# Kernel tuning notes

Measured on AMD Instinct MI355X. Metric: run time of the kernel, lower is better.

The kernel has to match this reference:

```python
import jax, jax.numpy as jnp
import numpy as np

NUM_GRAPHS = 256
NUM_LAYERS = 4
HIDDEN = 256
N_FEATS = 9
VOCAB = 119
BN_EPS = 1e-5


def setup_inputs() -> dict:
    key = jax.random.key(0)
    ks = jax.random.split(key, 16)
    N, E, H = 10000, 320000, HIDDEN
    x = jax.random.randint(ks[0], (N, N_FEATS), 0, 2, dtype=jnp.int64)
    edge_index = jax.random.randint(ks[1], (2, E), 0, N, dtype=jnp.int64)
    batch_ids = jnp.sort(jax.random.randint(ks[2], (N,), 0, NUM_GRAPHS, dtype=jnp.int64))
    s = 1.0 / np.sqrt(H)
    emb = jax.random.normal(ks[3], (N_FEATS, VOCAB, H), jnp.float32) * 0.02
    W = jax.random.normal(ks[4], (NUM_LAYERS, H, H), jnp.float32) * s
    b = jnp.zeros((NUM_LAYERS, H), jnp.float32)
    gamma = jnp.ones((NUM_LAYERS, H), jnp.float32)
    beta = jnp.zeros((NUM_LAYERS, H), jnp.float32)
    mlp_W1 = jax.random.normal(ks[5], (H, H // 2), jnp.float32) * s
    mlp_b1 = jnp.zeros((H // 2,), jnp.float32)
    mlp_W2 = jax.random.normal(ks[6], (H // 2, H // 4), jnp.float32) * (1.0 / np.sqrt(H // 2))
    mlp_b2 = jnp.zeros((H // 4,), jnp.float32)
    mlp_W3 = jax.random.normal(ks[7], (H // 4, 1), jnp.float32) * (1.0 / np.sqrt(H // 4))
    mlp_b3 = jnp.zeros((1,), jnp.float32)
    return dict(x=x, edge_index=edge_index, batch_ids=batch_ids, emb=emb, W=W, b=b,
                gamma=gamma, beta=beta, mlp_W1=mlp_W1, mlp_b1=mlp_b1,
                mlp_W2=mlp_W2, mlp_b2=mlp_b2, mlp_W3=mlp_W3, mlp_b3=mlp_b3)


def reference(x, edge_index, batch_ids, emb, W, b, gamma, beta,
              mlp_W1, mlp_b1, mlp_W2, mlp_b2, mlp_W3, mlp_b3):
    N = x.shape[0]
    src, dst = edge_index[0], edge_index[1]

    # AtomEncoder: sum of per-feature embeddings. emb[f, x[:,f]] -> [N, 9, H]
    h = jnp.sum(emb[jnp.arange(N_FEATS), x], axis=1)

    # GCN normalization with self-loops: deg_i = 1 + in-degree, norm = deg^-1/2
    deg = 1.0 + jax.ops.segment_sum(jnp.ones_like(dst, jnp.float32), dst, num_segments=N)
    nrm = jax.lax.rsqrt(deg)
    edge_w = (nrm[src] * nrm[dst])[:, None]   # [E,1]
    self_w = (nrm * nrm)[:, None]             # [N,1]

    for l in range(NUM_LAYERS):
        identity = h
        hw = h @ W[l]                                     # dense GEMM [N,H]x[H,H]
        agg = jax.ops.segment_sum(hw[src] * edge_w, dst, num_segments=N) + hw * self_w
        h = agg + b[l]
        # BatchNorm1d (training statistics over nodes)
        mu = jnp.mean(h, axis=0)
        var = jnp.var(h, axis=0)
        h = (h - mu) * jax.lax.rsqrt(var + BN_EPS) * gamma[l] + beta[l]
        h = jax.nn.relu(h)
        h = h + identity  # residual

    # global mean pool over graph ids
    sums = jax.ops.segment_sum(h, batch_ids, num_segments=NUM_GRAPHS)
    cnt = jax.ops.segment_sum(jnp.ones((N,), jnp.float32), batch_ids, num_segments=NUM_GRAPHS)
    g = sums / jnp.maximum(cnt, 1.0)[:, None]             # [G, H]

    # MLP head [H, H/2, H/4, 1]
    g = jax.nn.relu(g @ mlp_W1 + mlp_b1)
    g = jax.nn.relu(g @ mlp_W2 + mlp_b2)
    return g @ mlp_W3 + mlp_b3
```

## Files before the change

### kernel.cpp

```cpp
#include <hip/hip_runtime.h>

#define HID 256
#define NFEAT 9
#define VOCAB 119
#define NLAYERS 4
#define NGRAPHS 256
#define BN_EPS 1e-5f
#define POISON 0xAAAAAAAAu
#define CAP 128

typedef short short8 __attribute__((ext_vector_type(8)));
typedef float floatx4 __attribute__((ext_vector_type(4)));

__device__ inline unsigned short f2bf(float f) {
    unsigned int u = __float_as_uint(f);
    unsigned int r = u + 0x7FFF + ((u >> 16) & 1);
    return (unsigned short)(r >> 16);
}
__device__ inline float bf2f(unsigned short u) {
    return __uint_as_float(((unsigned int)u) << 16);
}

__global__ __launch_bounds__(256) void setup_misc(
        const int* __restrict__ x, const float* __restrict__ emb,
        const float* __restrict__ W, const int* __restrict__ src,
        const int* __restrict__ dst,
        int* __restrict__ fillc, int* __restrict__ bucket,
        unsigned short* __restrict__ wt, unsigned short* __restrict__ hbA,
        int N, int E, int nbFill) {
    const int bx = blockIdx.x;
    const int tid = threadIdx.x;
    __shared__ float sw[32][33];
    __shared__ int xf[NFEAT];

    if (bx < nbFill) {
        int i = bx * 256 + tid;
        if (i < E) {
            int d = dst[i];
            int slot = (int)((unsigned)atomicAdd(&fillc[d], 1) - POISON);
            if (slot < CAP) bucket[(size_t)d * CAP + slot] = src[i];
        }
    } else if (bx < nbFill + 256) {
        int j = bx - nbFill;
        int l = j >> 6;
        int rem = j & 63;
        int k0 = (rem >> 3) * 32, n0 = (rem & 7) * 32;
        int c = tid & 31, r8 = tid >> 5;
        const float* Wl = W + (size_t)l * HID * HID;
        unsigned short* Wtl = wt + (size_t)l * HID * HID;
#pragma unroll
        for (int p = 0; p < 4; ++p) {
            int r = r8 + p * 8;
            sw[r][c] = Wl[(k0 + r) * HID + n0 + c];
        }
        __syncthreads();
#pragma unroll
        for (int p = 0; p < 4; ++p) {
            int r = r8 + p * 8;
            Wtl[(size_t)(n0 + r) * HID + k0 + c] = f2bf(sw[c][r]);
        }
    } else {
        int n = bx - nbFill - 256;
        if (n < N) {
            if (tid < NFEAT) xf[tid] = x[n * NFEAT + tid];
            __syncthreads();
            float s = 0.f;
#pragma unroll
            for (int f = 0; f < NFEAT; ++f) s += emb[(size_t)(f * VOCAB + xf[f]) * HID + tid];
            hbA[(size_t)n * HID + tid] = f2bf(s);
        }
    }
}

__global__ __launch_bounds__(256) void agg_g4_kernel(const unsigned short* __restrict__ hb,
                                                     const int* __restrict__ fillc,
                                                     const int* __restrict__ bucket,
                                                     unsigned short* __restrict__ aggb, int N) {
    int bx = blockIdx.x;
    int half = bx & 1;
    int tid = threadIdx.x;
    int wave = tid >> 6;
    int lane = tid & 63;
    int g = lane >> 4;
    int sl = lane & 15;
    int n = (bx >> 1) * 4 + wave;
    if (n >= N) return;
    int co = half * 128 + sl * 8;
    const unsigned short* hbc = hb + co;
    int len = (int)((unsigned)fillc[n] - POISON);
    float nd = rsqrtf(1.0f + (float)len);
    int lenc = min(len, CAP);
    size_t bbase = (size_t)n * CAP;
    float a[8];
#pragma unroll
    for (int k = 0; k < 8; ++k) a[k] = 0.f;

    int done = 0;
    while (done < lenc) {
        int m = min(64, lenc - done);
        int li = done + (lane < m ? lane : m - 1);
        int sE = bucket[bbase + li];
        int dgs = (int)((unsigned)fillc[sE] - POISON);
        float wl = rsqrtf(1.0f + (float)dgs) * nd;
        int mq = m & ~3;
        int j = 0;
        for (; j < mq; j += 4) {
            int jj = j + g;
            int srcn = __shfl(sE, jj, 64);
            float w = __shfl(wl, jj, 64);
            short8 u = *(const short8*)&hbc[(size_t)srcn * HID];
#pragma unroll
            for (int k = 0; k < 8; ++k) a[k] += w * bf2f((unsigned short)u[k]);
        }
        if (j < m) {
            int jj = j + g;
            int cj = jj < m ? jj : (m - 1);
            int srcn = __shfl(sE, cj, 64);
            float w = __shfl(wl, cj, 64);
            if (jj >= m) w = 0.f;
            short8 u = *(const short8*)&hbc[(size_t)srcn * HID];
#pragma unroll
            for (int k = 0; k < 8; ++k) a[k] += w * bf2f((unsigned short)u[k]);
        }
        done += m;
    }
#pragma unroll
    for (int k = 0; k < 8; ++k) {
        a[k] += __shfl_xor(a[k], 16);
        a[k] += __shfl_xor(a[k], 32);
    }
    if (g == 0) {
        float sw2 = nd * nd;
        short8 us = *(const short8*)&hbc[(size_t)n * HID];
        short8 o;
#pragma unroll
        for (int k = 0; k < 8; ++k) {
            float v = a[k] + sw2 * bf2f((unsigned short)us[k]);
            o[k] = (short)f2bf(v);
        }
        *(short8*)&aggb[(size_t)n * HID + co] = o;
    }
}

__global__ __launch_bounds__(256) void mfma_gemm128(const unsigned short* __restrict__ A,
                                                    const unsigned short* __restrict__ Bt,
                                                    const float* __restrict__ bias,
                                                    unsigned short* __restrict__ C,
                                                    float* __restrict__ sums, int M) {
    __shared__ unsigned short As[128][40];
    __shared__ unsigned short Bs[64][40];
    __shared__ float lsum[64];
    __shared__ float lsq[64];
    int tid = threadIdx.x;
    int row0 = blockIdx.x * 128;
    int col0 = blockIdx.y * 64;
    int lane = tid & 63;
    int wid = tid >> 6;
    int arow = tid >> 1;
    int akc = (tid & 1) * 16;
    int brow = tid >> 2;
    int bkc = (tid & 3) * 8;
    int wm = (wid & 1) * 64;
    int wn = (wid >> 1) * 32;
    int quad = lane >> 4;
    int ln = lane & 15;

    floatx4 acc[4][2];
#pragma unroll
    for (int r = 0; r < 4; ++r)
#pragma unroll
        for (int c = 0; c < 2; ++c) acc[r][c] = (floatx4){0.f, 0.f, 0.f, 0.f};

    if (tid < 64) { lsum[tid] = 0.f; lsq[tid] = 0.f; }

    for (int kk = 0; kk < HID; kk += 32) {
        short8 av0 = {0, 0, 0, 0, 0, 0, 0, 0};
        short8 av1 = {0, 0, 0, 0, 0, 0, 0, 0};
        int ar = row0 + arow;
        if (ar < M) {
            av0 = *(const short8*)&A[(size_t)ar * HID + kk + akc];
            av1 = *(const short8*)&A[(size_t)ar * HID + kk + akc + 8];
        }
        short8 bv = *(const short8*)&Bt[(size_t)(col0 + brow) * HID + kk + bkc];
        *(short8*)&As[arow][akc] = av0;
        *(short8*)&As[arow][akc + 8] = av1;
        *(short8*)&Bs[brow][bkc] = bv;
        __syncthreads();
        short8 bf0 = *(const short8*)&Bs[wn + ln][quad * 8];
        short8 bf1 = *(const short8*)&Bs[wn + 16 + ln][quad * 8];
#pragma unroll
        for (int r = 0; r < 4; ++r) {
            short8 af = *(const short8*)&As[wm + r * 16 + ln][quad * 8];
            acc[r][0] = __builtin_amdgcn_mfma_f32_16x16x32_bf16(af, bf0, acc[r][0], 0, 0, 0);
            acc[r][1] = __builtin_amdgcn_mfma_f32_16x16x32_bf16(af, bf1, acc[r][1], 0, 0, 0);
        }
        __syncthreads();
    }
    float bias0 = bias[col0 + wn + ln];
    float bias1 = bias[col0 + wn + 16 + ln];
    float p0 = 0.f, q0 = 0.f, p1 = 0.f, q1 = 0.f;
#pragma unroll
    for (int r = 0; r < 4; ++r) {
#pragma unroll
        for (int rr = 0; rr < 4; ++rr) {
            int row = row0 + wm + r * 16 + quad * 4 + rr;
            if (row < M) {
                float v0 = acc[r][0][rr] + bias0;
                float v1 = acc[r][1][rr] + bias1;
                C[(size_t)row * HID + col0 + wn + ln] = f2bf(v0);
                C[(size_t)row * HID + col0 + wn + 16 + ln] = f2bf(v1);
                p0 += v0; q0 += v0 * v0;
                p1 += v1; q1 += v1 * v1;
            }
        }
    }
    atomicAdd(&lsum[wn + ln], p0);
    atomicAdd(&lsq[wn + ln], q0);
    atomicAdd(&lsum[wn + 16 + ln], p1);
    atomicAdd(&lsq[wn + 16 + ln], q1);
    __syncthreads();
    if (tid < 64) {
        unsafeAtomicAdd(&sums[col0 + tid], lsum[tid]);
        unsafeAtomicAdd(&sums[HID + col0 + tid], lsq[tid]);
    }
}

__global__ __launch_bounds__(256) void bn_kernel(const unsigned short* __restrict__ hwb,
                                                 const float* __restrict__ sums,
                                                 const float* __restrict__ gamma,
                                                 const float* __restrict__ beta,
                                                 const unsigned short* __restrict__ hold,
                                                 unsigned short* __restrict__ hbnew, int N) {
    int i4 = blockIdx.x * blockDim.x + threadIdx.x;
    int base = i4 * 4;
    if (base >= N * HID) return;
    int c = base & (HID - 1);
    float invN = 1.0f / (float)N;
    float4 s4 = *(const float4*)&sums[c];
    float4 q4 = *(const float4*)&sums[HID + c];
    float4 g4 = *(const float4*)&gamma[c];
    float4 be4 = *(const float4*)&beta[c];
    ushort4 v = *(const ushort4*)&hwb[base];
    ushort4 r = *(const ushort4*)&hold[base];
    ushort4 o;
    {
        float mu = s4.x * invN, var = q4.x * invN - mu * mu;
        o.x = f2bf(fmaxf((bf2f(v.x) - mu) * g4.x * rsqrtf(var + BN_EPS) + be4.x, 0.f) + bf2f(r.x));
        mu = s4.y * invN; var = q4.y * invN - mu * mu;
        o.y = f2bf(fmaxf((bf2f(v.y) - mu) * g4.y * rsqrtf(var + BN_EPS) + be4.y, 0.f) + bf2f(r.y));
        mu = s4.z * invN; var = q4.z * invN - mu * mu;
        o.z = f2bf(fmaxf((bf2f(v.z) - mu) * g4.z * rsqrtf(var + BN_EPS) + be4.z, 0.f) + bf2f(r.z));
        mu = s4.w * invN; var = q4.w * invN - mu * mu;
        o.w = f2bf(fmaxf((bf2f(v.w) - mu) * g4.w * rsqrtf(var + BN_EPS) + be4.w, 0.f) + bf2f(r.w));
    }
    *(ushort4*)&hbnew[base] = o;
}

__device__ inline int lower_bound_g(const int* __restrict__ a, int n, int key) {
    int lo = 0, hi = n;
    while (lo < hi) {
        int mid = (lo + hi) >> 1;
        if (a[mid] < key) lo = mid + 1; else hi = mid;
    }
    return lo;
}

__global__ __launch_bounds__(256) void pool_mlp_bn_kernel(
        const unsigned short* __restrict__ hwb,
        const float* __restrict__ sums,
        const float* __restrict__ gamma,
        const float* __restrict__ beta,
        const unsigned short* __restrict__ resid,
        const int* __restrict__ batch, int N,
        const float* __restrict__ W1, const float* __restrict__ b1,
        const float* __restrict__ W2, const float* __restrict__ b2,
        const float* __restrict__ W3, const float* __restrict__ b3,
        float* __restrict__ out) {
    int g = blockIdx.x, tid = threadIdx.x;
    int lo = lower_bound_g(batch, N, g);
    int hi = lower_bound_g(batch, N, g + 1);
    float invN = 1.0f / (float)N;
    float mu = sums[tid] * invN;
    float var = sums[HID + tid] * invN - mu * mu;
    float sc = gamma[tid] * rsqrtf(var + BN_EPS);
    float be = beta[tid];
    float s = 0.f;
    for (int i = lo; i < hi; ++i) {
        float v = (bf2f(hwb[(size_t)i * HID + tid]) - mu) * sc + be;
        v = fmaxf(v, 0.f) + bf2f(resid[(size_t)i * HID + tid]);
        s += v;
    }
    __shared__ float gs[256];
    __shared__ float t1[128];
    __shared__ float t2[64];
    float inv = 1.0f / fmaxf((float)(hi - lo), 1.0f);
    gs[tid] = s * inv;
    __syncthreads();
    if (tid < 128) {
        float a = b1[tid];
        for (int k = 0; k < 256; ++k) a += gs[k] * W1[k * 128 + tid];
        t1[tid] = fmaxf(a, 0.f);
    }
    __syncthreads();
    if (tid < 64) {
        float a = b2[tid];
        for (int k = 0; k < 128; ++k) a += t1[k] * W2[k * 64 + tid];
        t2[tid] = fmaxf(a, 0.f);
    }
    __syncthreads();
    if (tid < 64) {
        float p = t2[tid] * W3[tid];
#pragma unroll
        for (int off = 32; off >= 1; off >>= 1) p += __shfl_down(p, off);
        if (tid == 0) out[g] = p + b3[0];
    }
}

extern "C" void kernel_launch(void* const* d_in, const int* in_sizes, int n_in,
                              void* d_out, int out_size, void* d_ws, size_t ws_size,
                              hipStream_t stream) {
    const int* x      = (const int*)d_in[0];
    const int* ei     = (const int*)d_in[1];
    const int* batch  = (const int*)d_in[2];
    const float* emb  = (const float*)d_in[3];
    const float* W    = (const float*)d_in[4];
    const float* b    = (const float*)d_in[5];
    const float* gamma= (const float*)d_in[6];
    const float* beta = (const float*)d_in[7];
    const float* W1   = (const float*)d_in[8];
    const float* b1   = (const float*)d_in[9];
    const float* W2   = (const float*)d_in[10];
    const float* b2   = (const float*)d_in[11];
    const float* W3   = (const float*)d_in[12];
    const float* b3   = (const float*)d_in[13];
    float* out = (float*)d_out;

    int N = in_sizes[0] / NFEAT;
    int E = in_sizes[1] / 2;
    const int* srcp = ei;
    const int* dstp = ei + E;

    char* ws = (char*)d_ws;
    auto alloc = [&](size_t bytes) -> char* {
        char* p = ws;
        ws += (bytes + 255) & ~(size_t)255;
        return p;
    };
    int* fillc    = (int*)alloc((size_t)N * 4);
    int* bucket   = (int*)alloc((size_t)N * CAP * 4);
    unsigned short* hbA  = (unsigned short*)alloc((size_t)N * HID * 2);
    unsigned short* hbB  = (unsigned short*)alloc((size_t)N * HID * 2);
    unsigned short* aggb = (unsigned short*)alloc((size_t)N * HID * 2);
    unsigned short* hwb  = (unsigned short*)alloc((size_t)N * HID * 2);
    unsigned short* wt   = (unsigned short*)alloc((size_t)NLAYERS * HID * HID * 2);
    float* bnsums = (float*)alloc((size_t)NLAYERS * 2 * HID * 4);

    int nbFill = (E + 255) / 256;
    int miscGrid = nbFill + 256 + N;
    setup_misc<<<miscGrid, 256, 0, stream>>>(x, emb, W, srcp, dstp, fillc, bucket, wt, hbA,
                                             N, E, nbFill);

    unsigned short* hbcur = hbA;
    unsigned short* hboth = hbB;
    int aggGrid = ((N + 3) / 4) * 2;
    for (int l = 0; l < NLAYERS; ++l) {
        float* lsums = bnsums + (size_t)l * 2 * HID;
        agg_g4_kernel<<<aggGrid, 256, 0, stream>>>(hbcur, fillc, bucket, aggb, N);
        dim3 ggrid((N + 127) / 128, 4);
        mfma_gemm128<<<ggrid, 256, 0, stream>>>(aggb, wt + (size_t)l * HID * HID,
                                                b + (size_t)l * HID, hwb, lsums, N);
        if (l < NLAYERS - 1) {
            bn_kernel<<<((size_t)N * HID / 4 + 255) / 256, 256, 0, stream>>>(
                hwb, lsums, gamma + (size_t)l * HID, beta + (size_t)l * HID,
                hbcur, hboth, N);
            unsigned short* tb = hbcur; hbcur = hboth; hboth = tb;
        }
    }

    pool_mlp_bn_kernel<<<NGRAPHS, 256, 0, stream>>>(
        hwb, bnsums + (size_t)3 * 2 * HID, gamma + (size_t)3 * HID, beta + (size_t)3 * HID,
        hbcur, batch, N, W1, b1, W2, b2, W3, b3, out);
}
```

Before: 271.3 us.

## Fuse BatchNorm, ReLU and residual into GEMM epilogue via grid-wide column barrier

The separate BatchNorm kernel is removed. The GEMM now accumulates the column statistics, waits at a spin barrier until every row block of its column tile has contributed, then applies normalization, ReLU and the residual directly from its accumulators before writing the new hidden state. The bias add is also dropped, because batch-norm mean subtraction cancels it. This saves an extra read-write pass over the hidden activations and one launch per layer. In exchange, all blocks must be co-resident, which `launch_bounds(256,2)` is meant to ensure, and the barrier counter assumes the workspace starts at the poison value without being reset in-kernel.

```diff
diff --git a/kernel.cpp b/kernel.cpp
--- a/kernel.cpp
+++ b/kernel.cpp
@@ -142,11 +142,16 @@
     }
 }
 
-__global__ __launch_bounds__(256) void mfma_gemm128(const unsigned short* __restrict__ A,
-                                                    const unsigned short* __restrict__ Bt,
-                                                    const float* __restrict__ bias,
-                                                    unsigned short* __restrict__ C,
-                                                    float* __restrict__ sums, int M) {
+template <bool APPLY>
+__global__ __launch_bounds__(256, 2) void mfma_gemm_bn(
+        const unsigned short* __restrict__ A,
+        const unsigned short* __restrict__ Bt,
+        unsigned short* __restrict__ C,
+        float* __restrict__ sums,
+        const float* __restrict__ gamma,
+        const float* __restrict__ beta,
+        const unsigned short* __restrict__ resid,
+        int* __restrict__ cnt, int M) {
     __shared__ unsigned short As[128][40];
     __shared__ unsigned short Bs[64][40];
     __shared__ float lsum[64];
@@ -196,8 +201,8 @@
         }
         __syncthreads();
     }
-    float bias0 = bias[col0 + wn + ln];
-    float bias1 = bias[col0 + wn + 16 + ln];
+    const int c0 = col0 + wn + ln;
+    const int c1 = col0 + wn + 16 + ln;
     float p0 = 0.f, q0 = 0.f, p1 = 0.f, q1 = 0.f;
 #pragma unroll
     for (int r = 0; r < 4; ++r) {
@@ -205,10 +210,12 @@
         for (int rr = 0; rr < 4; ++rr) {
             int row = row0 + wm + r * 16 + quad * 4 + rr;
             if (row < M) {
-                float v0 = acc[r][0][rr] + bias0;
-                float v1 = acc[r][1][rr] + bias1;
-                C[(size_t)row * HID + col0 + wn + ln] = f2bf(v0);
-                C[(size_t)row * HID + col0 + wn + 16 + ln] = f2bf(v1);
+                float v0 = acc[r][0][rr];
+                float v1 = acc[r][1][rr];
+                if (!APPLY) {
+                    C[(size_t)row * HID + c0] = f2bf(v0);
+                    C[(size_t)row * HID + c1] = f2bf(v1);
+                }
                 p0 += v0; q0 += v0 * v0;
                 p1 += v1; q1 += v1 * v1;
             }
@@ -223,37 +230,43 @@
         unsafeAtomicAdd(&sums[col0 + tid], lsum[tid]);
         unsafeAtomicAdd(&sums[HID + col0 + tid], lsq[tid]);
     }
-}
-
-__global__ __launch_bounds__(256) void bn_kernel(const unsigned short* __restrict__ hwb,
-                                                 const float* __restrict__ sums,
-                                                 const float* __restrict__ gamma,
-                                                 const float* __restrict__ beta,
-                                                 const unsigned short* __restrict__ hold,
-                                                 unsigned short* __restrict__ hbnew, int N) {
-    int i4 = blockIdx.x * blockDim.x + threadIdx.x;
-    int base = i4 * 4;
-    if (base >= N * HID) return;
-    int c = base & (HID - 1);
-    float invN = 1.0f / (float)N;
-    float4 s4 = *(const float4*)&sums[c];
-    float4 q4 = *(const float4*)&sums[HID + c];
-    float4 g4 = *(const float4*)&gamma[c];
-    float4 be4 = *(const float4*)&beta[c];
-    ushort4 v = *(const ushort4*)&hwb[base];
-    ushort4 r = *(const ushort4*)&hold[base];
-    ushort4 o;
-    {
-        float mu = s4.x * invN, var = q4.x * invN - mu * mu;
-        o.x = f2bf(fmaxf((bf2f(v.x) - mu) * g4.x * rsqrtf(var + BN_EPS) + be4.x, 0.f) + bf2f(r.x));
-        mu = s4.y * invN; var = q4.y * invN - mu * mu;
-        o.y = f2bf(fmaxf((bf2f(v.y) - mu) * g4.y * rsqrtf(var + BN_EPS) + be4.y, 0.f) + bf2f(r.y));
-        mu = s4.z * invN; var = q4.z * invN - mu * mu;
-        o.z = f2bf(fmaxf((bf2f(v.z) - mu) * g4.z * rsqrtf(var + BN_EPS) + be4.z, 0.f) + bf2f(r.z));
-        mu = s4.w * invN; var = q4.w * invN - mu * mu;
-        o.w = f2bf(fmaxf((bf2f(v.w) - mu) * g4.w * rsqrtf(var + BN_EPS) + be4.w, 0.f) + bf2f(r.w));
-    }
-    *(ushort4*)&hbnew[base] = o;
+    if (APPLY) {
+        __syncthreads();
+        if (tid == 0) {
+            __threadfence();
+            atomicAdd(&cnt[blockIdx.y], 1);
+            unsigned target = gridDim.x;
+            while ((unsigned)__hip_atomic_load(&cnt[blockIdx.y], __ATOMIC_RELAXED,
+                                               __HIP_MEMORY_SCOPE_AGENT) - POISON < target)
+                __builtin_amdgcn_s_sleep(8);
+            __threadfence();
+        }
+        __syncthreads();
+        float invM = 1.0f / (float)M;
+        float s0 = __hip_atomic_load(&sums[c0], __ATOMIC_RELAXED, __HIP_MEMORY_SCOPE_AGENT);
+        float z0 = __hip_atomic_load(&sums[HID + c0], __ATOMIC_RELAXED, __HIP_MEMORY_SCOPE_AGENT);
+        float s1 = __hip_atomic_load(&sums[c1], __ATOMIC_RELAXED, __HIP_MEMORY_SCOPE_AGENT);
+        float z1 = __hip_atomic_load(&sums[HID + c1], __ATOMIC_RELAXED, __HIP_MEMORY_SCOPE_AGENT);
+        float mu0 = s0 * invM, var0 = z0 * invM - mu0 * mu0;
+        float mu1 = s1 * invM, var1 = z1 * invM - mu1 * mu1;
+        float sc0 = gamma[c0] * rsqrtf(var0 + BN_EPS), be0 = beta[c0];
+        float sc1 = gamma[c1] * rsqrtf(var1 + BN_EPS), be1 = beta[c1];
+#pragma unroll
+        for (int r = 0; r < 4; ++r) {
+#pragma unroll
+            for (int rr = 0; rr < 4; ++rr) {
+                int row = row0 + wm + r * 16 + quad * 4 + rr;
+                if (row < M) {
+                    float h0 = fmaxf((acc[r][0][rr] - mu0) * sc0 + be0, 0.f)
+                               + bf2f(resid[(size_t)row * HID + c0]);
+                    float h1 = fmaxf((acc[r][1][rr] - mu1) * sc1 + be1, 0.f)
+                               + bf2f(resid[(size_t)row * HID + c1]);
+                    C[(size_t)row * HID + c0] = f2bf(h0);
+                    C[(size_t)row * HID + c1] = f2bf(h1);
+                }
+            }
+        }
+    }
 }
 
 __device__ inline int lower_bound_g(const int* __restrict__ a, int n, int key) {
@@ -324,7 +337,6 @@
     const int* batch  = (const int*)d_in[2];
     const float* emb  = (const float*)d_in[3];
     const float* W    = (const float*)d_in[4];
-    const float* b    = (const float*)d_in[5];
     const float* gamma= (const float*)d_in[6];
     const float* beta = (const float*)d_in[7];
     const float* W1   = (const float*)d_in[8];
@@ -354,6 +366,7 @@
     unsigned short* hwb  = (unsigned short*)alloc((size_t)N * HID * 2);
     unsigned short* wt   = (unsigned short*)alloc((size_t)NLAYERS * HID * HID * 2);
     float* bnsums = (float*)alloc((size_t)NLAYERS * 2 * HID * 4);
+    int* cnt      = (int*)alloc((size_t)NLAYERS * 4 * 4);
 
     int nbFill = (E + 255) / 256;
     int miscGrid = nbFill + 256 + N;
@@ -363,17 +376,20 @@
     unsigned short* hbcur = hbA;
     unsigned short* hboth = hbB;
     int aggGrid = ((N + 3) / 4) * 2;
+    dim3 ggrid((N + 127) / 128, 4);
     for (int l = 0; l < NLAYERS; ++l) {
         float* lsums = bnsums + (size_t)l * 2 * HID;
         agg_g4_kernel<<<aggGrid, 256, 0, stream>>>(hbcur, fillc, bucket, aggb, N);
-        dim3 ggrid((N + 127) / 128, 4);
-        mfma_gemm128<<<ggrid, 256, 0, stream>>>(aggb, wt + (size_t)l * HID * HID,
-                                                b + (size_t)l * HID, hwb, lsums, N);
         if (l < NLAYERS - 1) {
-            bn_kernel<<<((size_t)N * HID / 4 + 255) / 256, 256, 0, stream>>>(
-                hwb, lsums, gamma + (size_t)l * HID, beta + (size_t)l * HID,
-                hbcur, hboth, N);
+            mfma_gemm_bn<true><<<ggrid, 256, 0, stream>>>(
+                aggb, wt + (size_t)l * HID * HID, hboth, lsums,
+                gamma + (size_t)l * HID, beta + (size_t)l * HID,
+                hbcur, cnt + l * 4, N);
             unsigned short* tb = hbcur; hbcur = hboth; hboth = tb;
+        } else {
+            mfma_gemm_bn<false><<<ggrid, 256, 0, stream>>>(
+                aggb, wt + (size_t)l * HID * HID, hwb, lsums,
+                nullptr, nullptr, nullptr, nullptr, N);
         }
     }
 
```

After: 323.2 us. 19.1% more time.

## Fuse all stages into one cooperative persistent kernel with grid syncs

Applied to the files above, without the earlier changes.

Replaces the sequence of separate launches (setup, per-layer aggregation, GEMM, batchnorm, pool+MLP) with one cooperative persistent kernel that loops over work units and separates stages with grid-wide syncs, falling back to the old launches if the cooperative launch fails. Shared memory is unioned across stages. This is meant to remove per-launch overhead and inter-kernel gaps. It also drops the bias add from the GEMM epilogue, which relies on batchnorm cancelling a per-column constant (the bias is zero in the test anyway). The risk is that grid syncs and a grid capped by occupancy limit parallelism in the gather and GEMM stages.

```diff
diff --git a/kernel.cpp b/kernel.cpp
--- a/kernel.cpp
+++ b/kernel.cpp
@@ -1,4 +1,7 @@
 #include <hip/hip_runtime.h>
+#include <hip/hip_cooperative_groups.h>
+
+namespace cg = cooperative_groups;
 
 #define HID 256
 #define NFEAT 9
@@ -21,69 +24,70 @@
     return __uint_as_float(((unsigned int)u) << 16);
 }
 
-__global__ __launch_bounds__(256) void setup_misc(
+struct SmemSetup { float sw[32][33]; int xf[NFEAT]; };
+struct SmemGemm  { unsigned short As[128][40]; unsigned short Bs[64][40];
+                   float lsum[64]; float lsq[64]; };
+struct SmemPool  { float gs[256]; float t1[128]; float t2[64]; };
+union SmemAll { SmemSetup s; SmemGemm g; SmemPool p; };
+
+__device__ inline void dev_setup_unit(int u, int tid,
         const int* __restrict__ x, const float* __restrict__ emb,
         const float* __restrict__ W, const int* __restrict__ src,
-        const int* __restrict__ dst,
-        int* __restrict__ fillc, int* __restrict__ bucket,
-        unsigned short* __restrict__ wt, unsigned short* __restrict__ hbA,
-        int N, int E, int nbFill) {
-    const int bx = blockIdx.x;
-    const int tid = threadIdx.x;
-    __shared__ float sw[32][33];
-    __shared__ int xf[NFEAT];
-
-    if (bx < nbFill) {
-        int i = bx * 256 + tid;
+        const int* __restrict__ dst, int* __restrict__ fillc,
+        int* __restrict__ bucket, unsigned short* __restrict__ wt,
+        unsigned short* __restrict__ hbA, int N, int E, int nbFill,
+        SmemSetup& sm) {
+    if (u < nbFill) {
+        int i = u * 256 + tid;
         if (i < E) {
             int d = dst[i];
             int slot = (int)((unsigned)atomicAdd(&fillc[d], 1) - POISON);
             if (slot < CAP) bucket[(size_t)d * CAP + slot] = src[i];
         }
-    } else if (bx < nbFill + 256) {
-        int j = bx - nbFill;
+    } else if (u < nbFill + 256) {
+        int j = u - nbFill;
         int l = j >> 6;
         int rem = j & 63;
         int k0 = (rem >> 3) * 32, n0 = (rem & 7) * 32;
         int c = tid & 31, r8 = tid >> 5;
         const float* Wl = W + (size_t)l * HID * HID;
         unsigned short* Wtl = wt + (size_t)l * HID * HID;
+        __syncthreads();
 #pragma unroll
         for (int p = 0; p < 4; ++p) {
             int r = r8 + p * 8;
-            sw[r][c] = Wl[(k0 + r) * HID + n0 + c];
+            sm.sw[r][c] = Wl[(k0 + r) * HID + n0 + c];
         }
         __syncthreads();
 #pragma unroll
         for (int p = 0; p < 4; ++p) {
             int r = r8 + p * 8;
-            Wtl[(size_t)(n0 + r) * HID + k0 + c] = f2bf(sw[c][r]);
+            Wtl[(size_t)(n0 + r) * HID + k0 + c] = f2bf(sm.sw[c][r]);
         }
     } else {
-        int n = bx - nbFill - 256;
+        int n = u - nbFill - 256;
         if (n < N) {
-            if (tid < NFEAT) xf[tid] = x[n * NFEAT + tid];
+            __syncthreads();
+            if (tid < NFEAT) sm.xf[tid] = x[n * NFEAT + tid];
             __syncthreads();
             float s = 0.f;
 #pragma unroll
-            for (int f = 0; f < NFEAT; ++f) s += emb[(size_t)(f * VOCAB + xf[f]) * HID + tid];
+            for (int f = 0; f < NFEAT; ++f)
+                s += emb[(size_t)(f * VOCAB + sm.xf[f]) * HID + tid];
             hbA[(size_t)n * HID + tid] = f2bf(s);
         }
     }
 }
 
-__global__ __launch_bounds__(256) void agg_g4_kernel(const unsigned short* __restrict__ hb,
-                                                     const int* __restrict__ fillc,
-                                                     const int* __restrict__ bucket,
-                                                     unsigned short* __restrict__ aggb, int N) {
-    int bx = blockIdx.x;
-    int half = bx & 1;
-    int tid = threadIdx.x;
+__device__ inline void dev_agg_unit(int u, int tid,
+        const unsigned short* __restrict__ hb, const int* __restrict__ fillc,
+        const int* __restrict__ bucket, unsigned short* __restrict__ aggb, int N) {
+    int half = u & 1;
     int wave = tid >> 6;
     int lane = tid & 63;
     int g = lane >> 4;
     int sl = lane & 15;
-    int n = (bx >> 1) * 4 + wave;
+    int n = (u >> 1) * 4 + wave;
     if (n >= N) return;
     int co = half * 128 + sl * 8;
     const unsigned short* hbc = hb + co;
@@ -108,9 +112,9 @@
             int jj = j + g;
             int srcn = __shfl(sE, jj, 64);
             float w = __shfl(wl, jj, 64);
-            short8 u = *(const short8*)&hbc[(size_t)srcn * HID];
-#pragma unroll
-            for (int k = 0; k < 8; ++k) a[k] += w * bf2f((unsigned short)u[k]);
+            short8 uvec = *(const short8*)&hbc[(size_t)srcn * HID];
+#pragma unroll
+            for (int k = 0; k < 8; ++k) a[k] += w * bf2f((unsigned short)uvec[k]);
         }
         if (j < m) {
             int jj = j + g;
@@ -118,9 +122,9 @@
             int srcn = __shfl(sE, cj, 64);
             float w = __shfl(wl, cj, 64);
             if (jj >= m) w = 0.f;
-            short8 u = *(const short8*)&hbc[(size_t)srcn * HID];
-#pragma unroll
-            for (int k = 0; k < 8; ++k) a[k] += w * bf2f((unsigned short)u[k]);
+            short8 uvec = *(const short8*)&hbc[(size_t)srcn * HID];
+#pragma unroll
+            for (int k = 0; k < 8; ++k) a[k] += w * bf2f((unsigned short)uvec[k]);
         }
         done += m;
     }
@@ -142,18 +146,12 @@
     }
 }
 
-__global__ __launch_bounds__(256) void mfma_gemm128(const unsigned short* __restrict__ A,
-                                                    const unsigned short* __restrict__ Bt,
-                                                    const float* __restrict__ bias,
-                                                    unsigned short* __restrict__ C,
-                                                    float* __restrict__ sums, int M) {
-    __shared__ unsigned short As[128][40];
-    __shared__ unsigned short Bs[64][40];
-    __shared__ float lsum[64];
-    __shared__ float lsq[64];
-    int tid = threadIdx.x;
-    int row0 = blockIdx.x * 128;
-    int col0 = blockIdx.y * 64;
+__device__ inline void dev_gemm_unit(int bxt, int by, int tid,
+        const unsigned short* __restrict__ A, const unsigned short* __restrict__ Bt,
+        unsigned short* __restrict__ C, float* __restrict__ sums,
+        SmemGemm& sm, int M) {
+    int row0 = bxt * 128;
+    int col0 = by * 64;
     int lane = tid & 63;
     int wid = tid >> 6;
     int arow = tid >> 1;
@@ -171,7 +169,7 @@
 #pragma unroll
         for (int c = 0; c < 2; ++c) acc[r][c] = (floatx4){0.f, 0.f, 0.f, 0.f};
 
-    if (tid < 64) { lsum[tid] = 0.f; lsq[tid] = 0.f; }
+    if (tid < 64) { sm.lsum[tid] = 0.f; sm.lsq[tid] = 0.f; }
 
     for (int kk = 0; kk < HID; kk += 32) {
         short8 av0 = {0, 0, 0, 0, 0, 0, 0, 0};
@@ -182,22 +180,22 @@
             av1 = *(const short8*)&A[(size_t)ar * HID + kk + akc + 8];
         }
         short8 bv = *(const short8*)&Bt[(size_t)(col0 + brow) * HID + kk + bkc];
-        *(short8*)&As[arow][akc] = av0;
-        *(short8*)&As[arow][akc + 8] = av1;
-        *(short8*)&Bs[brow][bkc] = bv;
+        *(short8*)&sm.As[arow][akc] = av0;
+        *(short8*)&sm.As[arow][akc + 8] = av1;
+        *(short8*)&sm.Bs[brow][bkc] = bv;
         __syncthreads();
-        short8 bf0 = *(const short8*)&Bs[wn + ln][quad * 8];
-        short8 bf1 = *(const short8*)&Bs[wn + 16 + ln][quad * 8];
+        short8 bf0 = *(const short8*)&sm.Bs[wn + ln][quad * 8];
+        short8 bf1 = *(const short8*)&sm.Bs[wn + 16 + ln][quad * 8];
 #pragma unroll
         for (int r = 0; r < 4; ++r) {
-            short8 af = *(const short8*)&As[wm + r * 16 + ln][quad * 8];
+            short8 af = *(const short8*)&sm.As[wm + r * 16 + ln][quad * 8];
             acc[r][0] = __builtin_amdgcn_mfma_f32_16x16x32_bf16(af, bf0, acc[r][0], 0, 0, 0);
             acc[r][1] = __builtin_amdgcn_mfma_f32_16x16x32_bf16(af, bf1, acc[r][1], 0, 0, 0);
         }
         __syncthreads();
     }
-    float bias0 = bias[col0 + wn + ln];
-    float bias1 = bias[col0 + wn + 16 + ln];
+    const int c0 = col0 + wn + ln;
+    const int c1 = col0 + wn + 16 + ln;
     float p0 = 0.f, q0 = 0.f, p1 = 0.f, q1 = 0.f;
 #pragma unroll
     for (int r = 0; r < 4; ++r) {
@@ -205,33 +203,32 @@
         for (int rr = 0; rr < 4; ++rr) {
             int row = row0 + wm + r * 16 + quad * 4 + rr;
             if (row < M) {
-                float v0 = acc[r][0][rr] + bias0;
-                float v1 = acc[r][1][rr] + bias1;
-                C[(size_t)row * HID + col0 + wn + ln] = f2bf(v0);
-                C[(size_t)row * HID + col0 + wn + 16 + ln] = f2bf(v1);
+                float v0 = acc[r][0][rr];
+                float v1 = acc[r][1][rr];
+                C[(size_t)row * HID + c0] = f2bf(v0);
+                C[(size_t)row * HID + c1] = f2bf(v1);
                 p0 += v0; q0 += v0 * v0;
                 p1 += v1; q1 += v1 * v1;
             }
         }
     }
-    atomicAdd(&lsum[wn + ln], p0);
-    atomicAdd(&lsq[wn + ln], q0);
-    atomicAdd(&lsum[wn + 16 + ln], p1);
-    atomicAdd(&lsq[wn + 16 + ln], q1);
+    atomicAdd(&sm.lsum[wn + ln], p0);
+    atomicAdd(&sm.lsq[wn + ln], q0);
+    atomicAdd(&sm.lsum[wn + 16 + ln], p1);
+    atomicAdd(&sm.lsq[wn + 16 + ln], q1);
     __syncthreads();
     if (tid < 64) {
-        unsafeAtomicAdd(&sums[col0 + tid], lsum[tid]);
-        unsafeAtomicAdd(&sums[HID + col0 + tid], lsq[tid]);
-    }
-}
-
-__global__ __launch_bounds__(256) void bn_kernel(const unsigned short* __restrict__ hwb,
-                                                 const float* __restrict__ sums,
-                                                 const float* __restrict__ gamma,
-                                                 const float* __restrict__ beta,
-                                                 const unsigned short* __restrict__ hold,
-                                                 unsigned short* __restrict__ hbnew, int N) {
-    int i4 = blockIdx.x * blockDim.x + threadIdx.x;
+        unsafeAtomicAdd(&sums[col0 + tid], sm.lsum[tid]);
+        unsafeAtomicAdd(&sums[HID + col0 + tid], sm.lsq[tid]);
+    }
+}
+
+__device__ inline void dev_bn_unit(int u, int tid,
+        const unsigned short* __restrict__ hwb, const float* __restrict__ sums,
+        const float* __restrict__ gamma, const float* __restrict__ beta,
+        const unsigned short* __restrict__ hold, unsigned short* __restrict__ hbnew,
+        int N) {
+    int i4 = u * 256 + tid;
     int base = i4 * 4;
     if (base >= N * HID) return;
     int c = base & (HID - 1);
@@ -265,18 +262,14 @@
     return lo;
 }
 
-__global__ __launch_bounds__(256) void pool_mlp_bn_kernel(
-        const unsigned short* __restrict__ hwb,
-        const float* __restrict__ sums,
-        const float* __restrict__ gamma,
-        const float* __restrict__ beta,
-        const unsigned short* __restrict__ resid,
-        const int* __restrict__ batch, int N,
+__device__ inline void dev_pool_unit(int g, int tid,
+        const unsigned short* __restrict__ hwb, const float* __restrict__ sums,
+        const float* __restrict__ gamma, const float* __restrict__ beta,
+        const unsigned short* __restrict__ resid, const int* __restrict__ batch, int N,
         const float* __restrict__ W1, const float* __restrict__ b1,
         const float* __restrict__ W2, const float* __restrict__ b2,
         const float* __restrict__ W3, const float* __restrict__ b3,
-        float* __restrict__ out) {
-    int g = blockIdx.x, tid = threadIdx.x;
+        float* __restrict__ out, SmemPool& sm) {
     int lo = lower_bound_g(batch, N, g);
     int hi = lower_bound_g(batch, N, g + 1);
     float invN = 1.0f / (float)N;
@@ -290,30 +283,132 @@
         v = fmaxf(v, 0.f) + bf2f(resid[(size_t)i * HID + tid]);
         s += v;
     }
-    __shared__ float gs[256];
-    __shared__ float t1[128];
-    __shared__ float t2[64];
     float inv = 1.0f / fmaxf((float)(hi - lo), 1.0f);
-    gs[tid] = s * inv;
+    sm.gs[tid] = s * inv;
     __syncthreads();
     if (tid < 128) {
         float a = b1[tid];
-        for (int k = 0; k < 256; ++k) a += gs[k] * W1[k * 128 + tid];
-        t1[tid] = fmaxf(a, 0.f);
+        for (int k = 0; k < 256; ++k) a += sm.gs[k] * W1[k * 128 + tid];
+        sm.t1[tid] = fmaxf(a, 0.f);
     }
     __syncthreads();
     if (tid < 64) {
         float a = b2[tid];
-        for (int k = 0; k < 128; ++k) a += t1[k] * W2[k * 64 + tid];
-        t2[tid] = fmaxf(a, 0.f);
+        for (int k = 0; k < 128; ++k) a += sm.t1[k] * W2[k * 64 + tid];
+        sm.t2[tid] = fmaxf(a, 0.f);
     }
     __syncthreads();
     if (tid < 64) {
-        float p = t2[tid] * W3[tid];
+        float p = sm.t2[tid] * W3[tid];
 #pragma unroll
         for (int off = 32; off >= 1; off >>= 1) p += __shfl_down(p, off);
         if (tid == 0) out[g] = p + b3[0];
     }
+}
+
+__global__ __launch_bounds__(256, 2) void mega_kernel(
+        const int* __restrict__ x, const int* __restrict__ src,
+        const int* __restrict__ dst, const int* __restrict__ batch,
+        const float* __restrict__ emb, const float* __restrict__ W,
+        const float* __restrict__ gamma, const float* __restrict__ beta,
+        const float* __restrict__ W1, const float* __restrict__ b1,
+        const float* __restrict__ W2, const float* __restrict__ b2,
+        const float* __restrict__ W3, const float* __restrict__ b3,
+        int* __restrict__ fillc, int* __restrict__ bucket,
+        unsigned short* __restrict__ hbA, unsigned short* __restrict__ hbB,
+        unsigned short* __restrict__ aggb, unsigned short* __restrict__ hwb,
+        unsigned short* __restrict__ wt, float* __restrict__ bnsums,
+        float* __restrict__ out, int N, int E) {
+    __shared__ SmemAll sm;
+    cg::grid_group gg = cg::this_grid();
+    const int bid = blockIdx.x, G = gridDim.x, tid = threadIdx.x;
+
+    const int nbFill = (E + 255) >> 8;
+    const int totalU0 = nbFill + 256 + N;
+    for (int u = bid; u < totalU0; u += G)
+        dev_setup_unit(u, tid, x, emb, W, src, dst, fillc, bucket, wt, hbA, N, E, nbFill, sm.s);
+    gg.sync();
+
+    unsigned short* hcur = hbA;
+    unsigned short* hoth = hbB;
+    const int aggU = ((N + 3) >> 2) * 2;
+    const int gx = (N + 127) >> 7;
+    for (int l = 0; l < NLAYERS; ++l) {
+        for (int u = bid; u < aggU; u += G)
+            dev_agg_unit(u, tid, hcur, fillc, bucket, aggb, N);
+        gg.sync();
+
+        const unsigned short* Bt = wt + (size_t)l * HID * HID;
+        float* lsums = bnsums + (size_t)l * 2 * HID;
+        for (int u = bid; u < gx * 4; u += G) {
+            int by = u / gx;
+            dev_gemm_unit(u - by * gx, by, tid, aggb, Bt, hwb, lsums, sm.g, N);
+            __syncthreads();
+        }
+        gg.sync();
+
+        if (l < NLAYERS - 1) {
+            const int bnU = (N * (HID / 4) + 255) >> 8;
+            for (int u = bid; u < bnU; u += G)
+                dev_bn_unit(u, tid, hwb, lsums, gamma + (size_t)l * HID,
+                            beta + (size_t)l * HID, hcur, hoth, N);
+            unsigned short* t = hcur; hcur = hoth; hoth = t;
+            gg.sync();
+        }
+    }
+
+    const float* l3sums = bnsums + (size_t)3 * 2 * HID;
+    for (int u = bid; u < NGRAPHS; u += G) {
+        dev_pool_unit(u, tid, hwb, l3sums, gamma + (size_t)3 * HID,
+                      beta + (size_t)3 * HID, hcur, batch, N,
+                      W1, b1, W2, b2, W3, b3, out, sm.p);
+        __syncthreads();
+    }
+}
+
+__global__ __launch_bounds__(256) void k_setup(
+        const int* __restrict__ x, const float* __restrict__ emb,
+        const float* __restrict__ W, const int* __restrict__ src,
+        const int* __restrict__ dst, int* __restrict__ fillc,
+        int* __restrict__ bucket, unsigned short* __restrict__ wt,
+        unsigned short* __restrict__ hbA, int N, int E, int nbFill) {
+    __shared__ SmemSetup sm;
+    dev_setup_unit(blockIdx.x, threadIdx.x, x, emb, W, src, dst, fillc, bucket, wt,
+                   hbA, N, E, nbFill, sm);
+}
+
+__global__ __launch_bounds__(256) void k_agg(
+        const unsigned short* __restrict__ hb, const int* __restrict__ fillc,
+        const int* __restrict__ bucket, unsigned short* __restrict__ aggb, int N) {
+    dev_agg_unit(blockIdx.x, threadIdx.x, hb, fillc, bucket, aggb, N);
+}
+
+__global__ __launch_bounds__(256) void k_gemm(
+        const unsigned short* __restrict__ A, const unsigned short* __restrict__ Bt,
+        unsigned short* __restrict__ C, float* __restrict__ sums, int M) {
+    __shared__ SmemGemm sm;
+    dev_gemm_unit(blockIdx.x, blockIdx.y, threadIdx.x, A, Bt, C, sums, sm, M);
+}
+
+__global__ __launch_bounds__(256) void k_bn(
+        const unsigned short* __restrict__ hwb, const float* __restrict__ sums,
+        const float* __restrict__ gamma, const float* __restrict__ beta,
+        const unsigned short* __restrict__ hold, unsigned short* __restrict__ hbnew,
+        int N) {
+    dev_bn_unit(blockIdx.x, threadIdx.x, hwb, sums, gamma, beta, hold, hbnew, N);
+}
+
+__global__ __launch_bounds__(256) void k_pool(
+        const unsigned short* __restrict__ hwb, const float* __restrict__ sums,
+        const float* __restrict__ gamma, const float* __restrict__ beta,
+        const unsigned short* __restrict__ resid, const int* __restrict__ batch, int N,
+        const float* __restrict__ W1, const float* __restrict__ b1,
+        const float* __restrict__ W2, const float* __restrict__ b2,
+        const float* __restrict__ W3, const float* __restrict__ b3,
+        float* __restrict__ out) {
+    __shared__ SmemPool sm;
+    dev_pool_unit(blockIdx.x, threadIdx.x, hwb, sums, gamma, beta, resid, batch, N,
+                  W1, b1, W2, b2, W3, b3, out, sm);
 }
 
 extern "C" void kernel_launch(void* const* d_in, const int* in_sizes, int n_in,
@@ -324,7 +419,6 @@
     const int* batch  = (const int*)d_in[2];
     const float* emb  = (const float*)d_in[3];
     const float* W    = (const float*)d_in[4];
-    const float* b    = (const float*)d_in[5];
     const float* gamma= (const float*)d_in[6];
     const float* beta = (const float*)d_in[7];
     const float* W1   = (const float*)d_in[8];
@@ -356,28 +450,53 @@
     float* bnsums = (float*)alloc((size_t)NLAYERS * 2 * HID * 4);
 
     int nbFill = (E + 255) / 256;
+
+    int maxB = 0;
+    hipError_t qerr = hipOccupancyMaxActiveBlocksPerMultiprocessor(
+        &maxB, (const void*)mega_kernel, 256, 0);
+    if (qerr != hipSuccess || maxB < 1) { maxB = 1; (void)hipGetLastError(); }
+    long grid = (long)maxB * 256;
+    if (grid > 2048) grid = 2048;
+    if (grid < 256) grid = 256;
+
+    void* args[] = { (void*)&x, (void*)&srcp, (void*)&dstp, (void*)&batch,
+                     (void*)&emb, (void*)&W, (void*)&gamma, (void*)&beta,
+                     (void*)&W1, (void*)&b1, (void*)&W2, (void*)&b2,
+                     (void*)&W3, (void*)&b3,
+                     (void*)&fillc, (void*)&bucket, (void*)&hbA, (void*)&hbB,
+                     (void*)&aggb, (void*)&hwb, (void*)&wt, (void*)&bnsums,
+                     (void*)&out, (void*)&N, (void*)&E };
+    hipError_t lerr = hipLaunchCooperativeKernel((const void*)mega_kernel,
+                                                 dim3((unsigned)grid), dim3(256),
+                                                 args, 0, stream);
+    if (lerr == hipSuccess) return;
+    (void)hipGetLastError();
+    if (grid > 256) {
+        lerr = hipLaunchCooperativeKernel((const void*)mega_kernel,
+                                          dim3(256), dim3(256), args, 0, stream);
+        if (lerr == hipSuccess) return;
+        (void)hipGetLastError();
+    }
+
     int miscGrid = nbFill + 256 + N;
-    setup_misc<<<miscGrid, 256, 0, stream>>>(x, emb, W, srcp, dstp, fillc, bucket, wt, hbA,
-                                             N, E, nbFill);
-
+    k_setup<<<miscGrid, 256, 0, stream>>>(x, emb, W, srcp, dstp, fillc, bucket, wt,
+                                          hbA, N, E, nbFill);
     unsigned short* hbcur = hbA;
     unsigned short* hboth = hbB;
     int aggGrid = ((N + 3) / 4) * 2;
+    dim3 ggrid((N + 127) / 128, 4);
     for (int l = 0; l < NLAYERS; ++l) {
         float* lsums = bnsums + (size_t)l * 2 * HID;
-        agg_g4_kernel<<<aggGrid, 256, 0, stream>>>(hbcur, fillc, bucket, aggb, N);
-        dim3 ggrid((N + 127) / 128, 4);
-        mfma_gemm128<<<ggrid, 256, 0, stream>>>(aggb, wt + (size_t)l * HID * HID,
-                                                b + (size_t)l * HID, hwb, lsums, N);
+        k_agg<<<aggGrid, 256, 0, stream>>>(hbcur, fillc, bucket, aggb, N);
+        k_gemm<<<ggrid, 256, 0, stream>>>(aggb, wt + (size_t)l * HID * HID, hwb, lsums, N);
         if (l < NLAYERS - 1) {
-            bn_kernel<<<((size_t)N * HID / 4 + 255) / 256, 256, 0, stream>>>(
+            k_bn<<<((size_t)N * HID / 4 + 255) / 256, 256, 0, stream>>>(
                 hwb, lsums, gamma + (size_t)l * HID, beta + (size_t)l * HID,
                 hbcur, hboth, N);
             unsigned short* tb = hbcur; hbcur = hboth; hboth = tb;
         }
     }
-
-    pool_mlp_bn_kernel<<<NGRAPHS, 256, 0, stream>>>(
-        hwb, bnsums + (size_t)3 * 2 * HID, gamma + (size_t)3 * HID, beta + (size_t)3 * HID,
-        hbcur, batch, N, W1, b1, W2, b2, W3, b3, out);
-}
+    k_pool<<<NGRAPHS, 256, 0, stream>>>(
+        hwb, bnsums + (size_t)3 * 2 * HID, gamma + (size_t)3 * HID,
+        beta + (size_t)3 * HID, hbcur, batch, N, W1, b1, W2, b2, W3, b3, out);
+}
```

Result: slower. 1.055 ms (+288.8%).

## Cache per-edge normalization weights across layers and drop pre-BatchNorm bias

Applied to the files above, without the earlier changes.

The first aggregation layer computes each edge's GCN weight, which needs a dependent gather of the source degree plus an rsqrt. It stores these weights in a per-node bucket-shaped buffer, and later layers read them back directly. The first chunk of bucket indices and weights is loaded up front, before the edge count is decoded, to shorten the dependent load chain. The GEMM no longer adds the layer bias, since training-mode BatchNorm subtracts the column mean and cancels it exactly. The cost is an extra N×CAP float workspace plus the writes to fill it in layer 0.

```diff
diff --git a/kernel.cpp b/kernel.cpp
--- a/kernel.cpp
+++ b/kernel.cpp
@@ -72,9 +72,11 @@
     }
 }
 
+template <bool FIRST>
 __global__ __launch_bounds__(256) void agg_g4_kernel(const unsigned short* __restrict__ hb,
                                                      const int* __restrict__ fillc,
                                                      const int* __restrict__ bucket,
+                                                     float* __restrict__ wbuf,
                                                      unsigned short* __restrict__ aggb, int N) {
     int bx = blockIdx.x;
     int half = bx & 1;
@@ -87,21 +89,24 @@
     if (n >= N) return;
     int co = half * 128 + sl * 8;
     const unsigned short* hbc = hb + co;
-    int len = (int)((unsigned)fillc[n] - POISON);
-    float nd = rsqrtf(1.0f + (float)len);
+    size_t bbase = (size_t)n * CAP;
+
+    int lenr = fillc[n];
+    int sE0 = bucket[bbase + lane];
+    float w0 = 0.f;
+    if (!FIRST) w0 = wbuf[bbase + lane];
+
+    int len = (int)((unsigned)lenr - POISON);
     int lenc = min(len, CAP);
-    size_t bbase = (size_t)n * CAP;
+    float nd = 0.f, sw2;
+    if (FIRST) { nd = rsqrtf(1.0f + (float)len); sw2 = nd * nd; }
+    else       { sw2 = 1.0f / (1.0f + (float)len); }
+
     float a[8];
 #pragma unroll
     for (int k = 0; k < 8; ++k) a[k] = 0.f;
 
-    int done = 0;
-    while (done < lenc) {
-        int m = min(64, lenc - done);
-        int li = done + (lane < m ? lane : m - 1);
-        int sE = bucket[bbase + li];
-        int dgs = (int)((unsigned)fillc[sE] - POISON);
-        float wl = rsqrtf(1.0f + (float)dgs) * nd;
+    auto process = [&](int m, int sE, float wl) {
         int mq = m & ~3;
         int j = 0;
         for (; j < mq; j += 4) {
@@ -122,15 +127,45 @@
 #pragma unroll
             for (int k = 0; k < 8; ++k) a[k] += w * bf2f((unsigned short)u[k]);
         }
+    };
+
+    int done = 0;
+    if (lenc > 0) {
+        int m = min(64, lenc);
+        float wl;
+        if (FIRST) {
+            int sg = (lane < m) ? sE0 : 0;
+            int dg = (int)((unsigned)fillc[sg] - POISON);
+            wl = rsqrtf(1.0f + (float)dg) * nd;
+            if (half == 0 && lane < m) wbuf[bbase + lane] = wl;
+        } else {
+            wl = w0;
+        }
+        process(m, sE0, wl);
+        done = m;
+    }
+    while (done < lenc) {
+        int m = min(64, lenc - done);
+        int li = done + (lane < m ? lane : m - 1);
+        int sE = bucket[bbase + li];
+        float wl;
+        if (FIRST) {
+            int dg = (int)((unsigned)fillc[sE] - POISON);
+            wl = rsqrtf(1.0f + (float)dg) * nd;
+            if (half == 0 && lane < m) wbuf[bbase + li] = wl;
+        } else {
+            wl = wbuf[bbase + li];
+        }
+        process(m, sE, wl);
         done += m;
     }
+
 #pragma unroll
     for (int k = 0; k < 8; ++k) {
         a[k] += __shfl_xor(a[k], 16);
         a[k] += __shfl_xor(a[k], 32);
     }
     if (g == 0) {
-        float sw2 = nd * nd;
         short8 us = *(const short8*)&hbc[(size_t)n * HID];
         short8 o;
 #pragma unroll
@@ -144,7 +179,6 @@
 
 __global__ __launch_bounds__(256) void mfma_gemm128(const unsigned short* __restrict__ A,
                                                     const unsigned short* __restrict__ Bt,
-                                                    const float* __restrict__ bias,
                                                     unsigned short* __restrict__ C,
                                                     float* __restrict__ sums, int M) {
     __shared__ unsigned short As[128][40];
@@ -196,8 +230,8 @@
         }
         __syncthreads();
     }
-    float bias0 = bias[col0 + wn + ln];
-    float bias1 = bias[col0 + wn + 16 + ln];
+    const int c0 = col0 + wn + ln;
+    const int c1 = col0 + wn + 16 + ln;
     float p0 = 0.f, q0 = 0.f, p1 = 0.f, q1 = 0.f;
 #pragma unroll
     for (int r = 0; r < 4; ++r) {
@@ -205,10 +239,10 @@
         for (int rr = 0; rr < 4; ++rr) {
             int row = row0 + wm + r * 16 + quad * 4 + rr;
             if (row < M) {
-                float v0 = acc[r][0][rr] + bias0;
-                float v1 = acc[r][1][rr] + bias1;
-                C[(size_t)row * HID + col0 + wn + ln] = f2bf(v0);
-                C[(size_t)row * HID + col0 + wn + 16 + ln] = f2bf(v1);
+                float v0 = acc[r][0][rr];
+                float v1 = acc[r][1][rr];
+                C[(size_t)row * HID + c0] = f2bf(v0);
+                C[(size_t)row * HID + c1] = f2bf(v1);
                 p0 += v0; q0 += v0 * v0;
                 p1 += v1; q1 += v1 * v1;
             }
@@ -324,7 +358,6 @@
     const int* batch  = (const int*)d_in[2];
     const float* emb  = (const float*)d_in[3];
     const float* W    = (const float*)d_in[4];
-    const float* b    = (const float*)d_in[5];
     const float* gamma= (const float*)d_in[6];
     const float* beta = (const float*)d_in[7];
     const float* W1   = (const float*)d_in[8];
@@ -348,6 +381,7 @@
     };
     int* fillc    = (int*)alloc((size_t)N * 4);
     int* bucket   = (int*)alloc((size_t)N * CAP * 4);
+    float* wbuf   = (float*)alloc((size_t)N * CAP * 4);
     unsigned short* hbA  = (unsigned short*)alloc((size_t)N * HID * 2);
     unsigned short* hbB  = (unsigned short*)alloc((size_t)N * HID * 2);
     unsigned short* aggb = (unsigned short*)alloc((size_t)N * HID * 2);
@@ -363,12 +397,14 @@
     unsigned short* hbcur = hbA;
     unsigned short* hboth = hbB;
     int aggGrid = ((N + 3) / 4) * 2;
+    dim3 ggrid((N + 127) / 128, 4);
     for (int l = 0; l < NLAYERS; ++l) {
         float* lsums = bnsums + (size_t)l * 2 * HID;
-        agg_g4_kernel<<<aggGrid, 256, 0, stream>>>(hbcur, fillc, bucket, aggb, N);
-        dim3 ggrid((N + 127) / 128, 4);
-        mfma_gemm128<<<ggrid, 256, 0, stream>>>(aggb, wt + (size_t)l * HID * HID,
-                                                b + (size_t)l * HID, hwb, lsums, N);
+        if (l == 0)
+            agg_g4_kernel<true><<<aggGrid, 256, 0, stream>>>(hbcur, fillc, bucket, wbuf, aggb, N);
+        else
+            agg_g4_kernel<false><<<aggGrid, 256, 0, stream>>>(hbcur, fillc, bucket, wbuf, aggb, N);
+        mfma_gemm128<<<ggrid, 256, 0, stream>>>(aggb, wt + (size_t)l * HID * HID, hwb, lsums, N);
         if (l < NLAYERS - 1) {
             bn_kernel<<<((size_t)N * HID / 4 + 255) / 256, 256, 0, stream>>>(
                 hwb, lsums, gamma + (size_t)l * HID, beta + (size_t)l * HID,
```

Result: faster. 261.0 us (-3.8%).
